# Optimization experiments

Hardware: AMD Instinct MI355X
Metric: run time of the kernel (lower is better)

## Reference

```python
import math
import jax
import jax.numpy as jnp
import numpy as np

LMAX = 6                 # lmax
F8, F2 = 16, 64          # f_out//8, f_out//2 for f_out=128
DIM6 = sum((2 * l + 1) ** 2 for l in range(LMAX + 1))  # 455 = dim of so3_irreps(6)
NA = NB = NG = 16        # SO(3) activation grid (alpha, beta, gamma)
B, T, H, C = 32, 16, 4, 128


def _real_sh(lmax, xyz):
    # real spherical harmonics: (N,3) unit vectors -> (N,(lmax+1)^2), m=-l..l per l
    x, y, z = xyz[:, 0], xyz[:, 1], xyz[:, 2]
    st = np.sqrt(np.clip(1.0 - z * z, 0.0, None))
    phi = np.arctan2(y, x)
    n = xyz.shape[0]
    P = np.zeros((lmax + 1, lmax + 1, n))
    P[0, 0] = 1.0
    for m in range(1, lmax + 1):
        P[m, m] = -(2 * m - 1) * st * P[m - 1, m - 1]
    for m in range(lmax):
        P[m + 1, m] = (2 * m + 1) * z * P[m, m]
    for m in range(lmax + 1):
        for l in range(m + 2, lmax + 1):
            P[l, m] = ((2 * l - 1) * z * P[l - 1, m] - (l + m - 1) * P[l - 2, m]) / (l - m)
    cols = []
    for l in range(lmax + 1):
        for m in range(-l, l + 1):
            am = abs(m)
            K = math.sqrt((2 * l + 1) / (4 * math.pi) * math.factorial(l - am) / math.factorial(l + am))
            if m > 0:
                cols.append(math.sqrt(2.0) * K * np.cos(m * phi) * P[l, m])
            elif m < 0:
                cols.append(math.sqrt(2.0) * K * np.sin(am * phi) * P[l, am])
            else:
                cols.append(K * P[l, 0])
    return np.stack(cols, axis=-1)


def _flat_wigner(lmax, Rs):
    # component-normalized flat real Wigner-D basis: (G,3,3) -> (G, sum_l (2l+1)^2)
    # D_l(R) solved from Y_l(R x) = D_l(R) Y_l(x) by least squares in float64
    rng = np.random.default_rng(0)
    pts = rng.normal(size=(32, 3))
    pts /= np.linalg.norm(pts, axis=1, keepdims=True)
    Y = _real_sh(lmax, pts)                                     # (32,(lmax+1)^2)
    rp = np.einsum('gij,nj->gni', Rs, pts).reshape(-1, 3)
    Yr = _real_sh(lmax, rp).reshape(len(Rs), 32, -1)            # (G,32,(lmax+1)^2)
    blocks = []
    for l in range(lmax + 1):
        d = 2 * l + 1
        o = l * l
        Apinv = np.linalg.pinv(Y[:, o:o + d])                   # (d,32)
        D = np.einsum('kn,gnm->gmk', Apinv, Yr[:, :, o:o + d])  # (G,d,d)
        blocks.append(math.sqrt(d) * D.reshape(len(Rs), d * d))
    return np.concatenate(blocks, axis=-1)


def _rz(a):
    c, s = np.cos(a), np.sin(a)
    z, o = np.zeros_like(a), np.ones_like(a)
    return np.stack([np.stack([c, -s, z], -1), np.stack([s, c, z], -1), np.stack([z, z, o], -1)], -2)


def _ry(a):
    c, s = np.cos(a), np.sin(a)
    z, o = np.zeros_like(a), np.ones_like(a)
    return np.stack([np.stack([c, z, s], -1), np.stack([z, o, z], -1), np.stack([-s, z, c], -1)], -2)


def _so3_grid():
    # ZYZ Euler grid, Gauss-Legendre in beta; rotations (G,3,3) + Haar weights (G,) summing to 1
    nodes, wts = np.polynomial.legendre.leggauss(NB)
    betas = np.arccos(nodes)
    alphas = np.arange(NA) * 2 * np.pi / NA
    gammas = np.arange(NG) * 2 * np.pi / NG
    Aa, Bb, Cg = np.meshgrid(alphas, betas, gammas, indexing='ij')
    Rs = _rz(Aa.ravel()) @ _ry(Bb.ravel()) @ _rz(Cg.ravel())
    w = np.broadcast_to(wts[None, :, None], (NA, NB, NG)).ravel().copy()
    w *= (2 * np.pi / NA) * (2 * np.pi / NG) / (8 * np.pi ** 2)
    return Rs, w


def _ico_rotations():
    # the 60 rotations of the icosahedral group, generated by closure
    phi = (1.0 + 5.0 ** 0.5) / 2.0
    def rot(axis, ang):
        a = np.asarray(axis, dtype=np.float64)
        a = a / np.linalg.norm(a)
        K = np.array([[0.0, -a[2], a[1]], [a[2], 0.0, -a[0]], [-a[1], a[0], 0.0]])
        return np.eye(3) + math.sin(ang) * K + (1.0 - math.cos(ang)) * (K @ K)
    gens = [rot([0.0, 1.0, phi], 2.0 * np.pi / 5.0), rot([0.0, 0.0, 1.0], np.pi)]
    elems = [np.eye(3)]
    seen = {tuple(np.round(np.eye(3), 5).ravel())}
    frontier = list(elems)
    while frontier:
        nxt = []
        for R in frontier:
            for g in gens:
                Q = g @ R
                k = tuple(np.round(Q, 5).ravel())
                if k not in seen:
                    seen.add(k)
                    elems.append(Q)
                    nxt.append(Q)
        frontier = nxt
    return np.stack(elems)


def _equi_linear(xl, wl):
    # e3nn-style per-irrep linear: xl (...,f_in,u,m), wl (f_in,f_out,u,v); fan_in = f_in*u
    fan_in = wl.shape[0] * wl.shape[2]
    return jnp.einsum('...fum,fguv->...gvm', xl, wl) / np.sqrt(fan_in)


def _forward(x, trajectory, w1s, w1v, w2, D_in, D_outw, ico_wigners):
    b, t, _ = trajectory.shape
    # pack '1x0e+3x1e': scalar = traj[...,9], vectors = traj[...,:9]
    s = trajectory[..., 9][..., None, None, None]       # (b,t,f=1,u=1,m=1)
    v = trajectory[..., :9].reshape(b, t, 1, 3, 3)      # (b,t,f=1,u=3,m=3)
    h = jnp.concatenate([_equi_linear(s, w1s).reshape(b, t, F8, 1),
                         _equi_linear(v, w1v).reshape(b, t, F8, 9)], axis=-1)  # (b,t,16,10)
    # SO(3) activation: coeffs -> grid signal -> relu -> coeffs (lmax 1 -> 6)
    sig = jax.nn.relu(jnp.einsum('btci,gi->btcg', h, D_in))
    h = jnp.einsum('btcg,gi->btci', sig, D_outw)        # (b,t,16,455)
    # per-l equivariant linear, f 16 -> 64
    outs = []
    o = 0
    for l in range(LMAX + 1):
        d = 2 * l + 1
        xl = h[..., o:o + d * d].reshape(b, t, F8, d, d)
        outs.append(_equi_linear(xl, w2[l]).reshape(b, t, F2, d * d))
        o += d * d
    traj = jnp.concatenate(outs, axis=-1)               # (b,t,64,455)
    traj = jnp.einsum('bhcj,ij->bhci', traj, ico_wigners)  # sample on ico rotations
    xg = jnp.einsum('bhcj,ij->bhci', x, ico_wigners)
    return xg, traj


def setup_inputs():
    key = jax.random.key(0)
    ks = jax.random.split(key, 11)
    Rs, w = _so3_grid()
    D_in = _flat_wigner(1, Rs).astype(np.float32)                      # (G,10)
    D_outw = (_flat_wigner(LMAX, Rs) * w[:, None]).astype(np.float32)  # (G,455)
    ico = _flat_wigner(LMAX, _ico_rotations()).astype(np.float32)      # (60,455)
    inp = dict(
        x=jax.random.normal(ks[0], (B, H, C, DIM6), jnp.float32),
        trajectory=jax.random.normal(ks[1], (B, T, 10), jnp.float32),
        w1s=jax.random.normal(ks[2], (1, F8, 1, 1), jnp.float32),
        w1v=jax.random.normal(ks[3], (1, F8, 3, 3), jnp.float32),
        D_in=jnp.asarray(D_in),
        D_outw=jnp.asarray(D_outw),
        ico_wigners=jnp.asarray(ico),
    )
    for l in range(LMAX + 1):
        inp['w2_%d' % l] = jax.random.normal(ks[4 + l], (F8, F2, 2 * l + 1, 2 * l + 1), jnp.float32)
    return inp


def reference(x, trajectory, w1s, w1v, w2_0, w2_1, w2_2, w2_3, w2_4, w2_5, w2_6, D_in, D_outw, ico_wigners):
    w2 = [w2_0, w2_1, w2_2, w2_3, w2_4, w2_5, w2_6]
    return _forward(x, trajectory, w1s, w1v, w2, D_in, D_outw, ico_wigners)
```

## Files before the change

### kernel.cpp

```cpp
#include <hip/hip_runtime.h>
#include <math.h>


#define NBT  512
#define F8c  16
#define F2c  64
#define GJ   455
#define GG   4096
#define NICO 60
#define JP   512

typedef short bf16x8 __attribute__((ext_vector_type(8)));
typedef float f32x4  __attribute__((ext_vector_type(4)));
typedef unsigned int u32;
typedef unsigned short ushort;

struct W7 { const float* p[7]; };

__device__ __forceinline__ ushort f2bf(float f) {
  u32 u = __float_as_uint(f);
  return (ushort)((u + 0x7fffu + ((u >> 16) & 1u)) >> 16);
}

__device__ __forceinline__ int sel7(int l, int a0, int a1, int a2, int a3,
                                    int a4, int a5, int a6) {
  int r = a6;
  r = (l == 5) ? a5 : r; r = (l == 4) ? a4 : r; r = (l == 3) ? a3 : r;
  r = (l == 2) ? a2 : r; r = (l == 1) ? a1 : r; r = (l == 0) ? a0 : r;
  return r;
}
__device__ __forceinline__ float sel7f(int l, float a0, float a1, float a2,
                                       float a3, float a4, float a5, float a6) {
  float r = a6;
  r = (l == 5) ? a5 : r; r = (l == 4) ? a4 : r; r = (l == 3) ? a3 : r;
  r = (l == 2) ? a2 : r; r = (l == 1) ? a1 : r; r = (l == 0) ? a0 : r;
  return r;
}

__global__ __launch_bounds__(256) void k_pre(const float* __restrict__ traj,
                                             const float* __restrict__ w1s,
                                             const float* __restrict__ w1v,
                                             const float* __restrict__ ico,
                                             const float* __restrict__ Dout,
                                             W7 w2,
                                             float* __restrict__ h,
                                             ushort* __restrict__ icoB,
                                             ushort* __restrict__ icoBx,
                                             ushort* __restrict__ DoutBT,
                                             ushort* __restrict__ Abuf,
                                             ushort* __restrict__ Bbuf) {
  __shared__ float t[64][65];
  int b = blockIdx.x, tid = threadIdx.x;
  if (b < 2240) {
    ((uint4*)Abuf)[b * 256 + tid] = (uint4){0, 0, 0, 0};
  } else if (b < 2752) {
    int b2 = b - 2240;
    int jt = b2 & 7, kt = b2 >> 3;
    int tx = tid & 63, ty = tid >> 6;
    #pragma unroll
    for (int i = 0; i < 16; ++i) {
      int r = i * 4 + ty, j = jt * 64 + tx;
      t[r][tx] = (j < GJ) ? Dout[(size_t)(kt * 64 + r) * GJ + j] : 0.f;
    }
    __syncthreads();
    #pragma unroll
    for (int i = 0; i < 16; ++i) {
      int jl = i * 4 + ty;
      DoutBT[(size_t)(jt * 64 + jl) * GG + kt * 64 + tx] = f2bf(t[tx][jl]);
    }
  } else if (b < 4992) {
    int ee = (b - 2752) * 256 + tid;
    if (ee < 573440) {
      int l = (ee >= 4096) + (ee >= 16384) + (ee >= 57344) + (ee >= 114688) +
              (ee >= 225280) + (ee >= 360448);
      int base = sel7(l, 0, 4096, 16384, 57344, 114688, 225280, 360448);
      int d    = sel7(l, 1, 3, 5, 7, 9, 11, 13);
      int Kp   = sel7(l, 64, 64, 128, 128, 192, 192, 256);
      int local = ee - base;
      int row = local / Kp, kcol = local - row * Kp;
      int g2 = row / d, v = row - g2 * d;
      ushort val = 0;
      if (kcol < 16 * d) {
        int f = kcol / d, u = kcol - f * d;
        const float* wl = w2.p[l];
        float scl = rsqrtf(16.f * (float)d);
        val = f2bf(wl[(((size_t)f * 64 + g2) * d + u) * d + v] * scl);
      }
      Bbuf[ee] = val;
    }
  } else if (b < 5312) {
    int idx = (b - 4992) * 256 + tid;
    if (idx < NBT * 160) {
      int bt = idx / 160, r = idx % 160, c = r / 10, i = r % 10;
      const float* tr = traj + bt * 10;
      float val;
      if (i == 0) {
        val = tr[9] * w1s[c];
      } else {
        int k = i - 1, v = k / 3, m = k % 3;
        float s = 0.f;
        #pragma unroll
        for (int u = 0; u < 3; ++u) s = fmaf(tr[u * 3 + m], w1v[c * 9 + u * 3 + v], s);
        val = s * 0.57735026918962576f;
      }
      h[idx] = val;
    }
  } else if (b < 5440) {
    int e = (b - 5312) * 256 + tid;
    int i = e >> 9, k = e & 511;
    ushort val = 0;
    if (i < NICO && k < GJ) {
      int l = (k >= 1) + (k >= 10) + (k >= 35) + (k >= 84) + (k >= 165) + (k >= 286);
      int o = sel7(l, 0, 1, 10, 35, 84, 165, 286);
      int d = sel7(l, 1, 3, 5, 7, 9, 11, 13);
      float rcpd = sel7f(l, 1.f, 1.f / 3.f, 0.2f, 1.f / 7.f, 1.f / 9.f,
                         1.f / 11.f, 1.f / 13.f);
      int local = k - o;
      int m = (int)(((float)local + 0.5f) * rcpd);
      int v = local - m * d;
      val = f2bf(ico[i * GJ + o + v * d + m]);
    }
    icoB[e] = val;
  } else {
    int e = (b - 5440) * 256 + tid;
    int i = e >> 9, j = e & 511;
    icoBx[e] = (i < NICO && j < GJ) ? f2bf(ico[i * GJ + j]) : (ushort)0;
  }
}

__global__ __launch_bounds__(256) void k_sig(const float* __restrict__ h,
                                             const float* __restrict__ Din,
                                             ushort* __restrict__ sigb) {
  __shared__ float hs[160];
  int tid = threadIdx.x;
  int mb = blockIdx.y;
  int kt = blockIdx.x;
  if (tid < 160) hs[tid] = h[mb * 160 + tid];
  float dr[80];
  const float4* dp = (const float4*)(Din + (size_t)(kt * 2048 + tid * 8) * 10);
  #pragma unroll
  for (int q = 0; q < 20; ++q) {
    float4 v = dp[q];
    dr[q * 4 + 0] = v.x; dr[q * 4 + 1] = v.y; dr[q * 4 + 2] = v.z; dr[q * 4 + 3] = v.w;
  }
  __syncthreads();
  #pragma unroll
  for (int r = 0; r < 16; ++r) {
    float hv[10];
    #pragma unroll
    for (int i = 0; i < 10; ++i) hv[i] = hs[r * 10 + i];
    bf16x8 o;
    #pragma unroll
    for (int j = 0; j < 8; ++j) {
      float s = 0.f;
      #pragma unroll
      for (int i = 0; i < 10; ++i) s = fmaf(hv[i], dr[j * 10 + i], s);
      o[j] = (short)f2bf(fmaxf(s, 0.f));
    }
    *(bf16x8*)&sigb[((size_t)(mb * 16 + r)) * GG + kt * 2048 + tid * 8] = o;
  }
}

__global__ __launch_bounds__(256) void k_mm2s(const ushort* __restrict__ A,
                                              const ushort* __restrict__ Bm,
                                              float* __restrict__ part) {
  __shared__ __align__(16) short Asb[2][128 * 64];
  __shared__ __align__(16) short Bsb[2][128 * 64];
  int tid = threadIdx.x;
  int lane = tid & 63, wid = tid >> 6;
  int quad = lane >> 4, lr = lane & 15;
  int wm = wid >> 1, wn = wid & 1;
  int bid = blockIdx.x;
  int mb = bid & 63;
  int split = (bid >> 6) & 1;
  int nb = bid >> 7;
  int k0 = split * 2048;

  const ushort* Ab = A + (size_t)mb * 128 * GG + k0;
  const ushort* Bb = Bm + (size_t)nb * 128 * GG + k0;

  f32x4 acc[4][4];
  #pragma unroll
  for (int a = 0; a < 4; ++a)
    #pragma unroll
    for (int b = 0; b < 4; ++b) acc[a][b] = (f32x4){0.f, 0.f, 0.f, 0.f};

  auto stage = [&](int buf, int kc) {
    #pragma unroll
    for (int it = 0; it < 4; ++it) {
      int s0 = (wid * 4 + it) * 64;
      int s = s0 + lane;
      int r = s >> 3, pp = s & 7, p = pp ^ (r & 7);
      __builtin_amdgcn_global_load_lds(
          (const __attribute__((address_space(1))) u32*)(Ab + (size_t)r * GG + kc + p * 8),
          (__attribute__((address_space(3))) u32*)(&Asb[buf][s0 * 8]), 16, 0, 0);
    }
    #pragma unroll
    for (int it = 0; it < 4; ++it) {
      int s0 = (wid * 4 + it) * 64;
      int s = s0 + lane;
      int r = s >> 3, pp = s & 7, p = pp ^ (r & 7);
      __builtin_amdgcn_global_load_lds(
          (const __attribute__((address_space(1))) u32*)(Bb + (size_t)r * GG + kc + p * 8),
          (__attribute__((address_space(3))) u32*)(&Bsb[buf][s0 * 8]), 16, 0, 0);
    }
  };

  stage(0, 0);
  __syncthreads();
  for (int it = 0; it < 32; ++it) {
    int cur = it & 1;
    if (it < 31) stage(cur ^ 1, (it + 1) * 64);
    #pragma unroll
    for (int ks = 0; ks < 2; ++ks) {
      bf16x8 af[4], bv[4];
      #pragma unroll
      for (int mt = 0; mt < 4; ++mt) {
        int ra = wm * 64 + mt * 16 + lr;
        int v = (ks * 4 + quad) ^ (ra & 7);
        af[mt] = *(const bf16x8*)&Asb[cur][(ra * 8 + v) * 8];
      }
      #pragma unroll
      for (int nt = 0; nt < 4; ++nt) {
        int rb = wn * 64 + nt * 16 + lr;
        int v = (ks * 4 + quad) ^ (rb & 7);
        bv[nt] = *(const bf16x8*)&Bsb[cur][(rb * 8 + v) * 8];
      }
      #pragma unroll
      for (int mt = 0; mt < 4; ++mt)
        #pragma unroll
        for (int nt = 0; nt < 4; ++nt)
          acc[mt][nt] = __builtin_amdgcn_mfma_f32_16x16x32_bf16(af[mt], bv[nt], acc[mt][nt], 0, 0, 0);
    }
    __syncthreads();
  }
  #pragma unroll
  for (int mt = 0; mt < 4; ++mt)
    #pragma unroll
    for (int nt = 0; nt < 4; ++nt) {
      int j = nb * 128 + wn * 64 + nt * 16 + lr;
      #pragma unroll
      for (int r = 0; r < 4; ++r) {
        int m = mb * 128 + wm * 64 + mt * 16 + quad * 4 + r;
        part[((size_t)split * 8192 + m) * 512 + j] = acc[mt][nt][r];
      }
    }
}

__global__ __launch_bounds__(256) void k_red(const float* __restrict__ part,
                                             ushort* __restrict__ Abuf) {
  int t = blockIdx.x * 256 + threadIdx.x;
  int e0 = t * 8;
  int m = e0 >> 9, j0 = e0 & 511;
  const float4* p0 = (const float4*)(part + (size_t)m * 512 + j0);
  const float4* p1 = (const float4*)(part + (size_t)(8192 + m) * 512 + j0);
  float4 a0 = p0[0], a1 = p0[1], b0 = p1[0], b1 = p1[1];
  float s[8] = {a0.x + b0.x, a0.y + b0.y, a0.z + b0.z, a0.w + b0.w,
                a1.x + b1.x, a1.y + b1.y, a1.z + b1.z, a1.w + b1.w};
  int btg = m >> 4, f = m & 15;
  #pragma unroll
  for (int jj = 0; jj < 8; ++jj) {
    int j = j0 + jj;
    if (j < GJ) {
      int l = (j >= 1) + (j >= 10) + (j >= 35) + (j >= 84) + (j >= 165) + (j >= 286);
      int o    = sel7(l, 0, 1, 10, 35, 84, 165, 286);
      int d    = sel7(l, 1, 3, 5, 7, 9, 11, 13);
      int Kp   = sel7(l, 64, 64, 128, 128, 192, 192, 256);
      int Aoff = sel7(l, 0, 32768, 131072, 458752, 917504, 1802240, 2883584);
      float rcpd = sel7f(l, 1.f, 1.f / 3.f, 0.2f, 1.f / 7.f, 1.f / 9.f,
                         1.f / 11.f, 1.f / 13.f);
      int jl = j - o;
      int u = (int)(((float)jl + 0.5f) * rcpd);
      int mB = jl - u * d;
      Abuf[(size_t)Aoff + ((size_t)btg * d + mB) * Kp + f * d + u] = f2bf(s[jj]);
    }
  }
}

__global__ __launch_bounds__(256) void k_mm2f(const ushort* __restrict__ A,
                                              const ushort* __restrict__ Bm,
                                              ushort* __restrict__ Abuf) {
  __shared__ __align__(16) short Asb[2][128 * 64];
  __shared__ __align__(16) short Bsb[2][128 * 64];
  int tid = threadIdx.x;
  int lane = tid & 63, wid = tid >> 6;
  int quad = lane >> 4, lr = lane & 15;
  int wm = wid >> 1, wn = wid & 1;
  int bid = blockIdx.x;
  int mb = bid & 63, nb = bid >> 6;
  f32x4 acc[4][4];
  #pragma unroll
  for (int a = 0; a < 4; ++a)
    #pragma unroll
    for (int b = 0; b < 4; ++b) acc[a][b] = (f32x4){0.f, 0.f, 0.f, 0.f};
  const ushort* Ab = A + (size_t)mb * 128 * GG;
  const ushort* Bb = Bm + (size_t)nb * 128 * GG;
  auto stage = [&](int buf, int kc) {
    #pragma unroll
    for (int it = 0; it < 4; ++it) {
      int s0 = (wid * 4 + it) * 64;
      int s = s0 + lane;
      int r = s >> 3, pp = s & 7, p = pp ^ (r & 7);
      __builtin_amdgcn_global_load_lds(
          (const __attribute__((address_space(1))) u32*)(Ab + (size_t)r * GG + kc + p * 8),
          (__attribute__((address_space(3))) u32*)(&Asb[buf][s0 * 8]), 16, 0, 0);
    }
    #pragma unroll
    for (int it = 0; it < 4; ++it) {
      int s0 = (wid * 4 + it) * 64;
      int s = s0 + lane;
      int r = s >> 3, pp = s & 7, p = pp ^ (r & 7);
      __builtin_amdgcn_global_load_lds(
          (const __attribute__((address_space(1))) u32*)(Bb + (size_t)r * GG + kc + p * 8),
          (__attribute__((address_space(3))) u32*)(&Bsb[buf][s0 * 8]), 16, 0, 0);
    }
  };
  stage(0, 0);
  __syncthreads();
  for (int it = 0; it < 64; ++it) {
    int cur = it & 1;
    if (it < 63) stage(cur ^ 1, (it + 1) * 64);
    #pragma unroll
    for (int ks = 0; ks < 2; ++ks) {
      bf16x8 af[4], bvv[4];
      #pragma unroll
      for (int mt = 0; mt < 4; ++mt) {
        int ra = wm * 64 + mt * 16 + lr;
        int v = (ks * 4 + quad) ^ (ra & 7);
        af[mt] = *(const bf16x8*)&Asb[cur][(ra * 8 + v) * 8];
      }
      #pragma unroll
      for (int nt = 0; nt < 4; ++nt) {
        int rb = wn * 64 + nt * 16 + lr;
        int v = (ks * 4 + quad) ^ (rb & 7);
        bvv[nt] = *(const bf16x8*)&Bsb[cur][(rb * 8 + v) * 8];
      }
      #pragma unroll
      for (int mt = 0; mt < 4; ++mt)
        #pragma unroll
        for (int nt = 0; nt < 4; ++nt)
          acc[mt][nt] = __builtin_amdgcn_mfma_f32_16x16x32_bf16(af[mt], bvv[nt], acc[mt][nt], 0, 0, 0);
    }
    __syncthreads();
  }
  #pragma unroll
  for (int nt = 0; nt < 4; ++nt) {
    int j = nb * 128 + wn * 64 + nt * 16 + lr;
    if (j < GJ) {
      int l = (j >= 1) + (j >= 10) + (j >= 35) + (j >= 84) + (j >= 165) + (j >= 286);
      int o    = sel7(l, 0, 1, 10, 35, 84, 165, 286);
      int d    = sel7(l, 1, 3, 5, 7, 9, 11, 13);
      int Kp   = sel7(l, 64, 64, 128, 128, 192, 192, 256);
      int Aoff = sel7(l, 0, 32768, 131072, 458752, 917504, 1802240, 2883584);
      int jl = j - o;
      float rcpd = 1.0f / (float)d;
      int u = (int)(((float)jl + 0.5f) * rcpd);
      int mB = jl - u * d;
      #pragma unroll
      for (int mt = 0; mt < 4; ++mt)
        #pragma unroll
        for (int r = 0; r < 4; ++r) {
          int m = mb * 128 + wm * 64 + mt * 16 + quad * 4 + r;
          int btg = m >> 4, f = m & 15;
          Abuf[(size_t)Aoff + ((size_t)btg * d + mB) * Kp + f * d + u] =
              f2bf(acc[mt][nt][r]);
        }
    }
  }
}

__global__ __launch_bounds__(256) void k_batchX(const ushort* __restrict__ Abuf,
                                                const ushort* __restrict__ Bbuf,
                                                const float* __restrict__ x,
                                                const ushort* __restrict__ icoBx,
                                                ushort* __restrict__ trajbf,
                                                float* __restrict__ xg) {
  __shared__ __align__(16) short As[64 * 64];
  __shared__ __align__(16) short Bs[64 * 64];
  int bid = blockIdx.x;
  int tid = threadIdx.x;
  int lane = tid & 63, wid = tid >> 6;
  int quad = lane >> 4, lr = lane & 15;
  int wm = wid >> 1, wn = wid & 1;
  f32x4 acc[2][2];
  #pragma unroll
  for (int a = 0; a < 2; ++a)
    #pragma unroll
    for (int b = 0; b < 2; ++b) acc[a][b] = (f32x4){0.f, 0.f, 0.f, 0.f};

  if (bid >= 3640) {
    int mtile = bid - 3640;
    for (int kc = 0; kc < JP; kc += 64) {
      __syncthreads();
      #pragma unroll
      for (int it = 0; it < 2; ++it) {
        int s = it * 256 + tid;
        int r = s >> 3, p8 = s & 7, p = p8 ^ (r & 7);
        const float* xr = x + (size_t)(mtile * 64 + r) * GJ;
        int j0 = kc + p * 8;
        bf16x8 v8;
        #pragma unroll
        for (int jj = 0; jj < 8; ++jj) {
          int j = j0 + jj;
          v8[jj] = (j < GJ) ? (short)f2bf(xr[j]) : (short)0;
        }
        *(bf16x8*)&As[s * 8] = v8;
      }
      #pragma unroll
      for (int it = 0; it < 2; ++it) {
        int s0 = (wid * 2 + it) * 64;
        int s = s0 + lane;
        int r = s >> 3, p8 = s & 7, p = p8 ^ (r & 7);
        const ushort* gb = icoBx + (size_t)r * JP + kc + p * 8;
        __builtin_amdgcn_global_load_lds(
            (const __attribute__((address_space(1))) u32*)gb,
            (__attribute__((address_space(3))) u32*)(Bs + s0 * 8), 16, 0, 0);
      }
      __syncthreads();
      #pragma unroll
      for (int ks = 0; ks < 2; ++ks) {
        int v = (ks * 4 + quad) ^ (lr & 7);
        bf16x8 af[2], bfv[2];
        #pragma unroll
        for (int mt = 0; mt < 2; ++mt)
          af[mt] = *(const bf16x8*)&As[(wm * 32 + mt * 16 + lr) * 64 + v * 8];
        #pragma unroll
        for (int nt = 0; nt < 2; ++nt)
          bfv[nt] = *(const bf16x8*)&Bs[(wn * 32 + nt * 16 + lr) * 64 + v * 8];
        #pragma unroll
        for (int mt = 0; mt < 2; ++mt)
          #pragma unroll
          for (int nt = 0; nt < 2; ++nt)
            acc[mt][nt] = __builtin_amdgcn_mfma_f32_16x16x32_bf16(af[mt], bfv[nt], acc[mt][nt], 0, 0, 0);
      }
    }
    #pragma unroll
    for (int mt = 0; mt < 2; ++mt)
      #pragma unroll
      for (int nt = 0; nt < 2; ++nt) {
        int i = wn * 32 + nt * 16 + lr;
        if (i < NICO) {
          #pragma unroll
          for (int r = 0; r < 4; ++r) {
            int row = mtile * 64 + wm * 32 + mt * 16 + quad * 4 + r;
            xg[(size_t)row * NICO + i] = acc[mt][nt][r];
          }
        }
      }
    return;
  }

  int l = (bid >= 8) + (bid >= 80) + (bid >= 280) + (bid >= 672) +
          (bid >= 1320) + (bid >= 2288);
  int bbase = sel7(l, 0, 8, 80, 280, 672, 1320, 2288);
  int d     = sel7(l, 1, 3, 5, 7, 9, 11, 13);
  int Kp    = sel7(l, 64, 64, 128, 128, 192, 192, 256);
  int o     = sel7(l, 0, 1, 10, 35, 84, 165, 286);
  int Aoff  = sel7(l, 0, 32768, 131072, 458752, 917504, 1802240, 2883584);
  int Boff  = sel7(l, 0, 4096, 16384, 57344, 114688, 225280, 360448);
  int t = bid - bbase;
  float rcp8d = sel7f(l, 1.f / 8.f, 1.f / 24.f, 1.f / 40.f, 1.f / 56.f,
                      1.f / 72.f, 1.f / 88.f, 1.f / 104.f);
  int ntile = (int)(((float)t + 0.5f) * rcp8d);
  int mtile = t - ntile * 8 * d;

  const ushort* Ab = Abuf + Aoff;
  const ushort* Bb = Bbuf + Boff;

  for (int kc = 0; kc < Kp; kc += 64) {
    __syncthreads();
    #pragma unroll
    for (int it = 0; it < 2; ++it) {
      int s0 = (wid * 2 + it) * 64;
      int s = s0 + lane;
      int r = s >> 3, p8 = s & 7, p = p8 ^ (r & 7);
      const ushort* ga = Ab + (size_t)(mtile * 64 + r) * Kp + kc + p * 8;
      __builtin_amdgcn_global_load_lds(
          (const __attribute__((address_space(1))) u32*)ga,
          (__attribute__((address_space(3))) u32*)(As + s0 * 8), 16, 0, 0);
      const ushort* gb = Bb + (size_t)(ntile * 64 + r) * Kp + kc + p * 8;
      __builtin_amdgcn_global_load_lds(
          (const __attribute__((address_space(1))) u32*)gb,
          (__attribute__((address_space(3))) u32*)(Bs + s0 * 8), 16, 0, 0);
    }
    __syncthreads();
    #pragma unroll
    for (int ks = 0; ks < 2; ++ks) {
      int v = (ks * 4 + quad) ^ (lr & 7);
      bf16x8 af[2], bfv[2];
      #pragma unroll
      for (int mt = 0; mt < 2; ++mt)
        af[mt] = *(const bf16x8*)&As[(wm * 32 + mt * 16 + lr) * 64 + v * 8];
      #pragma unroll
      for (int nt = 0; nt < 2; ++nt)
        bfv[nt] = *(const bf16x8*)&Bs[(wn * 32 + nt * 16 + lr) * 64 + v * 8];
      #pragma unroll
      for (int mt = 0; mt < 2; ++mt)
        #pragma unroll
        for (int nt = 0; nt < 2; ++nt)
          acc[mt][nt] = __builtin_amdgcn_mfma_f32_16x16x32_bf16(af[mt], bfv[nt], acc[mt][nt], 0, 0, 0);
    }
  }
  #pragma unroll
  for (int mt = 0; mt < 2; ++mt)
    #pragma unroll
    for (int nt = 0; nt < 2; ++nt)
      #pragma unroll
      for (int r = 0; r < 4; ++r) {
        int Mrow = mtile * 64 + wm * 32 + mt * 16 + quad * 4 + r;
        int Ncol = ntile * 64 + wn * 32 + nt * 16 + lr;
        int bt = Mrow / d, m = Mrow - bt * d;
        int g2 = Ncol / d, v = Ncol - g2 * d;
        trajbf[(size_t)(bt * 64 + g2) * JP + o + m * d + v] = f2bf(acc[mt][nt][r]);
      }
}

__global__ __launch_bounds__(256) void k_icoT(const ushort* __restrict__ trajbf,
                                              const ushort* __restrict__ icoB,
                                              float* __restrict__ trajo) {
  __shared__ __align__(16) short As[64 * 64];
  __shared__ __align__(16) short Bs[64 * 64];
  int mtile = blockIdx.x;
  int tid = threadIdx.x;
  int lane = tid & 63, wid = tid >> 6;
  int quad = lane >> 4, lr = lane & 15;
  int wm = wid >> 1, wn = wid & 1;
  f32x4 acc[2][2];
  #pragma unroll
  for (int a = 0; a < 2; ++a)
    #pragma unroll
    for (int b = 0; b < 2; ++b) acc[a][b] = (f32x4){0.f, 0.f, 0.f, 0.f};
  for (int kc = 0; kc < JP; kc += 64) {
    __syncthreads();
    #pragma unroll
    for (int it = 0; it < 2; ++it) {
      int s0 = (wid * 2 + it) * 64;
      int s = s0 + lane;
      int r = s >> 3, p8 = s & 7, p = p8 ^ (r & 7);
      const ushort* ga = trajbf + (size_t)(mtile * 64 + r) * JP + kc + p * 8;
      __builtin_amdgcn_global_load_lds(
          (const __attribute__((address_space(1))) u32*)ga,
          (__attribute__((address_space(3))) u32*)(As + s0 * 8), 16, 0, 0);
      const ushort* gb = icoB + (size_t)r * JP + kc + p * 8;
      __builtin_amdgcn_global_load_lds(
          (const __attribute__((address_space(1))) u32*)gb,
          (__attribute__((address_space(3))) u32*)(Bs + s0 * 8), 16, 0, 0);
    }
    __syncthreads();
    #pragma unroll
    for (int ks = 0; ks < 2; ++ks) {
      int v = (ks * 4 + quad) ^ (lr & 7);
      bf16x8 af[2], bfv[2];
      #pragma unroll
      for (int mt = 0; mt < 2; ++mt)
        af[mt] = *(const bf16x8*)&As[(wm * 32 + mt * 16 + lr) * 64 + v * 8];
      #pragma unroll
      for (int nt = 0; nt < 2; ++nt)
        bfv[nt] = *(const bf16x8*)&Bs[(wn * 32 + nt * 16 + lr) * 64 + v * 8];
      #pragma unroll
      for (int mt = 0; mt < 2; ++mt)
        #pragma unroll
        for (int nt = 0; nt < 2; ++nt)
          acc[mt][nt] = __builtin_amdgcn_mfma_f32_16x16x32_bf16(af[mt], bfv[nt], acc[mt][nt], 0, 0, 0);
    }
  }
  #pragma unroll
  for (int mt = 0; mt < 2; ++mt)
    #pragma unroll
    for (int nt = 0; nt < 2; ++nt) {
      int i = wn * 32 + nt * 16 + lr;
      if (i < NICO) {
        #pragma unroll
        for (int r = 0; r < 4; ++r) {
          int row = mtile * 64 + wm * 32 + mt * 16 + quad * 4 + r;
          trajo[(size_t)row * NICO + i] = acc[mt][nt][r];
        }
      }
    }
}

extern "C" void kernel_launch(void* const* d_in, const int* in_sizes, int n_in,
                              void* d_out, int out_size, void* d_ws, size_t ws_size,
                              hipStream_t stream) {
  const float *x = nullptr, *traj = nullptr, *w1s = nullptr, *w1v = nullptr;
  const float *Din = nullptr, *Dout = nullptr, *ico = nullptr;
  W7 w2{};
  for (int i = 0; i < n_in; ++i) {
    const float* p = (const float*)d_in[i];
    switch (in_sizes[i]) {
      case 7454720: x = p; break;
      case 5120:    traj = p; break;
      case 16:      w1s = p; break;
      case 144:     w1v = p; break;
      case 40960:   Din = p; break;
      case 1863680: Dout = p; break;
      case 27300:   ico = p; break;
      case 1024:    w2.p[0] = p; break;
      case 9216:    w2.p[1] = p; break;
      case 25600:   w2.p[2] = p; break;
      case 50176:   w2.p[3] = p; break;
      case 82944:   w2.p[4] = p; break;
      case 123904:  w2.p[5] = p; break;
      case 173056:  w2.p[6] = p; break;
      default: break;
    }
  }
  char* wsb = (char*)d_ws;
  float*  h       = (float*)wsb;
  ushort* DoutBT  = (ushort*)(wsb + 327680);
  ushort* icoB    = (ushort*)(wsb + 4521984);
  ushort* icoBx   = (ushort*)(wsb + 4587520);
  ushort* Abuf    = (ushort*)(wsb + 4653056);
  ushort* Bbuf    = (ushort*)(wsb + 13828096);
  ushort* sigb    = (ushort*)(wsb + 14974976);
  ushort* trajbf  = sigb;
  float*  part    = (float*)(wsb + 82083840);
  float* xg    = (float*)d_out;
  float* trajo = (float*)d_out + 983040;

  k_pre<<<dim3(5568), dim3(256), 0, stream>>>(traj, w1s, w1v, ico, Dout, w2,
                                              h, icoB, icoBx, DoutBT, Abuf, Bbuf);
  k_sig<<<dim3(2, 512), dim3(256), 0, stream>>>(h, Din, sigb);
  if (ws_size >= 115638272ULL) {
    k_mm2s<<<dim3(512),  dim3(256), 0, stream>>>(sigb, DoutBT, part);
    k_red <<<dim3(2048), dim3(256), 0, stream>>>(part, Abuf);
  } else {
    k_mm2f<<<dim3(256),  dim3(256), 0, stream>>>(sigb, DoutBT, Abuf);
  }
  k_batchX<<<dim3(3896), dim3(256), 0, stream>>>(Abuf, Bbuf, x, icoBx, trajbf, xg);
  k_icoT  <<<dim3(512),  dim3(256), 0, stream>>>(trajbf, icoB, trajo);
}
```

Baseline: 231.3 us.

## Double-buffer LDS tiles in batched GEMM and ico projection kernels

Adds two LDS buffers for the A and B tiles in k_batchX and k_icoT. The next K-chunk is staged with global_load_lds, or for the x path loaded into registers and converted to bf16 after compute, while MFMAs run on the current chunk. The goal is to overlap global load latency with matrix math and drop one barrier per iteration. In exchange, LDS use per block doubles to 32KB, which may lower occupancy, and the x path holds 16 extra floats in registers.

```diff
diff --git a/kernel.cpp b/kernel.cpp
--- a/kernel.cpp
+++ b/kernel.cpp
@@ -375,8 +375,8 @@
                                                 const ushort* __restrict__ icoBx,
                                                 ushort* __restrict__ trajbf,
                                                 float* __restrict__ xg) {
-  __shared__ __align__(16) short As[64 * 64];
-  __shared__ __align__(16) short Bs[64 * 64];
+  __shared__ __align__(16) short As[2][64 * 64];
+  __shared__ __align__(16) short Bs[2][64 * 64];
   int bid = blockIdx.x;
   int tid = threadIdx.x;
   int lane = tid & 63, wid = tid >> 6;
@@ -388,24 +388,52 @@
     #pragma unroll
     for (int b = 0; b < 2; ++b) acc[a][b] = (f32x4){0.f, 0.f, 0.f, 0.f};
 
+  auto compute = [&](int cur) {
+    #pragma unroll
+    for (int ks = 0; ks < 2; ++ks) {
+      int v = (ks * 4 + quad) ^ (lr & 7);
+      bf16x8 af[2], bfv[2];
+      #pragma unroll
+      for (int mt = 0; mt < 2; ++mt)
+        af[mt] = *(const bf16x8*)&As[cur][(wm * 32 + mt * 16 + lr) * 64 + v * 8];
+      #pragma unroll
+      for (int nt = 0; nt < 2; ++nt)
+        bfv[nt] = *(const bf16x8*)&Bs[cur][(wn * 32 + nt * 16 + lr) * 64 + v * 8];
+      #pragma unroll
+      for (int mt = 0; mt < 2; ++mt)
+        #pragma unroll
+        for (int nt = 0; nt < 2; ++nt)
+          acc[mt][nt] = __builtin_amdgcn_mfma_f32_16x16x32_bf16(af[mt], bfv[nt], acc[mt][nt], 0, 0, 0);
+    }
+  };
+
   if (bid >= 3640) {
     int mtile = bid - 3640;
-    for (int kc = 0; kc < JP; kc += 64) {
-      __syncthreads();
-      #pragma unroll
-      for (int it = 0; it < 2; ++it) {
-        int s = it * 256 + tid;
+    auto loadx = [&](int itk, float* xv) {
+      #pragma unroll
+      for (int half = 0; half < 2; ++half) {
+        int s = half * 256 + tid;
         int r = s >> 3, p8 = s & 7, p = p8 ^ (r & 7);
         const float* xr = x + (size_t)(mtile * 64 + r) * GJ;
-        int j0 = kc + p * 8;
-        bf16x8 v8;
+        int j0 = itk * 64 + p * 8;
         #pragma unroll
         for (int jj = 0; jj < 8; ++jj) {
           int j = j0 + jj;
-          v8[jj] = (j < GJ) ? (short)f2bf(xr[j]) : (short)0;
+          xv[half * 8 + jj] = (j < GJ) ? xr[j] : 0.f;
         }
-        *(bf16x8*)&As[s * 8] = v8;
-      }
+      }
+    };
+    auto writex = [&](int buf, const float* xv) {
+      #pragma unroll
+      for (int half = 0; half < 2; ++half) {
+        int s = half * 256 + tid;
+        bf16x8 v8;
+        #pragma unroll
+        for (int jj = 0; jj < 8; ++jj) v8[jj] = (short)f2bf(xv[half * 8 + jj]);
+        *(bf16x8*)&As[buf][s * 8] = v8;
+      }
+    };
+    auto stageB = [&](int buf, int kc) {
       #pragma unroll
       for (int it = 0; it < 2; ++it) {
         int s0 = (wid * 2 + it) * 64;
@@ -414,25 +442,24 @@
         const ushort* gb = icoBx + (size_t)r * JP + kc + p * 8;
         __builtin_amdgcn_global_load_lds(
             (const __attribute__((address_space(1))) u32*)gb,
-            (__attribute__((address_space(3))) u32*)(Bs + s0 * 8), 16, 0, 0);
-      }
+            (__attribute__((address_space(3))) u32*)(&Bs[buf][s0 * 8]), 16, 0, 0);
+      }
+    };
+    float xv[16];
+    loadx(0, xv);
+    writex(0, xv);
+    stageB(0, 0);
+    __syncthreads();
+    for (int it = 0; it < 8; ++it) {
+      int cur = it & 1;
+      float xn[16];
+      if (it < 7) {
+        loadx(it + 1, xn);
+        stageB(cur ^ 1, (it + 1) * 64);
+      }
+      compute(cur);
+      if (it < 7) writex(cur ^ 1, xn);
       __syncthreads();
-      #pragma unroll
-      for (int ks = 0; ks < 2; ++ks) {
-        int v = (ks * 4 + quad) ^ (lr & 7);
-        bf16x8 af[2], bfv[2];
-        #pragma unroll
-        for (int mt = 0; mt < 2; ++mt)
-          af[mt] = *(const bf16x8*)&As[(wm * 32 + mt * 16 + lr) * 64 + v * 8];
-        #pragma unroll
-        for (int nt = 0; nt < 2; ++nt)
-          bfv[nt] = *(const bf16x8*)&Bs[(wn * 32 + nt * 16 + lr) * 64 + v * 8];
-        #pragma unroll
-        for (int mt = 0; mt < 2; ++mt)
-          #pragma unroll
-          for (int nt = 0; nt < 2; ++nt)
-            acc[mt][nt] = __builtin_amdgcn_mfma_f32_16x16x32_bf16(af[mt], bfv[nt], acc[mt][nt], 0, 0, 0);
-      }
     }
     #pragma unroll
     for (int mt = 0; mt < 2; ++mt)
@@ -467,8 +494,7 @@
   const ushort* Ab = Abuf + Aoff;
   const ushort* Bb = Bbuf + Boff;
 
-  for (int kc = 0; kc < Kp; kc += 64) {
-    __syncthreads();
+  auto stage = [&](int buf, int kc) {
     #pragma unroll
     for (int it = 0; it < 2; ++it) {
       int s0 = (wid * 2 + it) * 64;
@@ -477,29 +503,22 @@
       const ushort* ga = Ab + (size_t)(mtile * 64 + r) * Kp + kc + p * 8;
       __builtin_amdgcn_global_load_lds(
           (const __attribute__((address_space(1))) u32*)ga,
-          (__attribute__((address_space(3))) u32*)(As + s0 * 8), 16, 0, 0);
+          (__attribute__((address_space(3))) u32*)(&As[buf][s0 * 8]), 16, 0, 0);
       const ushort* gb = Bb + (size_t)(ntile * 64 + r) * Kp + kc + p * 8;
       __builtin_amdgcn_global_load_lds(
           (const __attribute__((address_space(1))) u32*)gb,
-          (__attribute__((address_space(3))) u32*)(Bs + s0 * 8), 16, 0, 0);
-    }
+          (__attribute__((address_space(3))) u32*)(&Bs[buf][s0 * 8]), 16, 0, 0);
+    }
+  };
+
+  int nIter = Kp >> 6;
+  stage(0, 0);
+  __syncthreads();
+  for (int it = 0; it < nIter; ++it) {
+    int cur = it & 1;
+    if (it + 1 < nIter) stage(cur ^ 1, (it + 1) * 64);
+    compute(cur);
     __syncthreads();
-    #pragma unroll
-    for (int ks = 0; ks < 2; ++ks) {
-      int v = (ks * 4 + quad) ^ (lr & 7);
-      bf16x8 af[2], bfv[2];
-      #pragma unroll
-      for (int mt = 0; mt < 2; ++mt)
-        af[mt] = *(const bf16x8*)&As[(wm * 32 + mt * 16 + lr) * 64 + v * 8];
-      #pragma unroll
-      for (int nt = 0; nt < 2; ++nt)
-        bfv[nt] = *(const bf16x8*)&Bs[(wn * 32 + nt * 16 + lr) * 64 + v * 8];
-      #pragma unroll
-      for (int mt = 0; mt < 2; ++mt)
-        #pragma unroll
-        for (int nt = 0; nt < 2; ++nt)
-          acc[mt][nt] = __builtin_amdgcn_mfma_f32_16x16x32_bf16(af[mt], bfv[nt], acc[mt][nt], 0, 0, 0);
-    }
   }
   #pragma unroll
   for (int mt = 0; mt < 2; ++mt)
@@ -518,8 +537,8 @@
 __global__ __launch_bounds__(256) void k_icoT(const ushort* __restrict__ trajbf,
                                               const ushort* __restrict__ icoB,
                                               float* __restrict__ trajo) {
-  __shared__ __align__(16) short As[64 * 64];
-  __shared__ __align__(16) short Bs[64 * 64];
+  __shared__ __align__(16) short As[2][64 * 64];
+  __shared__ __align__(16) short Bs[2][64 * 64];
   int mtile = blockIdx.x;
   int tid = threadIdx.x;
   int lane = tid & 63, wid = tid >> 6;
@@ -530,8 +549,8 @@
   for (int a = 0; a < 2; ++a)
     #pragma unroll
     for (int b = 0; b < 2; ++b) acc[a][b] = (f32x4){0.f, 0.f, 0.f, 0.f};
-  for (int kc = 0; kc < JP; kc += 64) {
-    __syncthreads();
+
+  auto stage = [&](int buf, int kc) {
     #pragma unroll
     for (int it = 0; it < 2; ++it) {
       int s0 = (wid * 2 + it) * 64;
@@ -540,29 +559,36 @@
       const ushort* ga = trajbf + (size_t)(mtile * 64 + r) * JP + kc + p * 8;
       __builtin_amdgcn_global_load_lds(
           (const __attribute__((address_space(1))) u32*)ga,
-          (__attribute__((address_space(3))) u32*)(As + s0 * 8), 16, 0, 0);
+          (__attribute__((address_space(3))) u32*)(&As[buf][s0 * 8]), 16, 0, 0);
       const ushort* gb = icoB + (size_t)r * JP + kc + p * 8;
       __builtin_amdgcn_global_load_lds(
           (const __attribute__((address_space(1))) u32*)gb,
-          (__attribute__((address_space(3))) u32*)(Bs + s0 * 8), 16, 0, 0);
-    }
-    __syncthreads();
+          (__attribute__((address_space(3))) u32*)(&Bs[buf][s0 * 8]), 16, 0, 0);
+    }
+  };
+
+  stage(0, 0);
+  __syncthreads();
+  for (int it = 0; it < 8; ++it) {
+    int cur = it & 1;
+    if (it < 7) stage(cur ^ 1, (it + 1) * 64);
     #pragma unroll
     for (int ks = 0; ks < 2; ++ks) {
       int v = (ks * 4 + quad) ^ (lr & 7);
       bf16x8 af[2], bfv[2];
       #pragma unroll
       for (int mt = 0; mt < 2; ++mt)
-        af[mt] = *(const bf16x8*)&As[(wm * 32 + mt * 16 + lr) * 64 + v * 8];
+        af[mt] = *(const bf16x8*)&As[cur][(wm * 32 + mt * 16 + lr) * 64 + v * 8];
       #pragma unroll
       for (int nt = 0; nt < 2; ++nt)
-        bfv[nt] = *(const bf16x8*)&Bs[(wn * 32 + nt * 16 + lr) * 64 + v * 8];
+        bfv[nt] = *(const bf16x8*)&Bs[cur][(wn * 32 + nt * 16 + lr) * 64 + v * 8];
       #pragma unroll
       for (int mt = 0; mt < 2; ++mt)
         #pragma unroll
         for (int nt = 0; nt < 2; ++nt)
           acc[mt][nt] = __builtin_amdgcn_mfma_f32_16x16x32_bf16(af[mt], bfv[nt], acc[mt][nt], 0, 0, 0);
     }
+    __syncthreads();
   }
   #pragma unroll
   for (int mt = 0; mt < 2; ++mt)
```

Result: no change. 232.7 us (+0.6%).
